# Kernel tuning notes

Measured on AMD Instinct MI355X. Metric: run time of the kernel, lower is better.

The kernel has to match this reference:

```python
import jax, jax.numpy as jnp
import numpy as np
import math

N_STFT = 1025
N_MELS = 128
SAMPLE_RATE = 16000
F_MIN = 0.0
F_MAX = 8000.0
MAX_ITER = 20
LR = 0.3
MOMENTUM = 0.9
BATCH = 4
TIME = 1024


def _create_fb_matrix(n_freqs, f_min, f_max, n_mels, sample_rate):
    # Triangular mel filterbank, (n_freqs, n_mels), matching torchaudio's create_fb_matrix.
    all_freqs = np.linspace(0.0, sample_rate // 2, n_freqs)
    m_min = 2595.0 * math.log10(1.0 + f_min / 700.0)
    m_max = 2595.0 * math.log10(1.0 + f_max / 700.0)
    m_pts = np.linspace(m_min, m_max, n_mels + 2)
    f_pts = 700.0 * (10.0 ** (m_pts / 2595.0) - 1.0)
    f_diff = f_pts[1:] - f_pts[:-1]
    slopes = f_pts[None, :] - all_freqs[:, None]  # (n_freqs, n_mels+2)
    down_slopes = -slopes[:, :-2] / f_diff[:-1]
    up_slopes = slopes[:, 2:] / f_diff[1:]
    fb = np.maximum(0.0, np.minimum(down_slopes, up_slopes))
    return jnp.asarray(fb, dtype=jnp.float32)


def setup_inputs() -> dict:
    key = jax.random.key(0)
    k1, k2 = jax.random.split(key)
    melspec = jax.random.uniform(k1, (BATCH, N_MELS, TIME), dtype=jnp.float32)
    # torch.rand initialization of the estimated spectrogram, exposed for determinism
    spec_init = jax.random.uniform(k2, (BATCH, TIME, N_STFT), dtype=jnp.float32)
    fb = _create_fb_matrix(N_STFT, F_MIN, F_MAX, N_MELS, SAMPLE_RATE)
    return {"melspec": melspec, "spec_init": spec_init, "fb": fb}


def reference(melspec, spec_init, fb):
    # melspec: (B, n_mels, T) -> (B, T, n_mels); fb: (n_stft, n_mels)
    mel_t = jnp.swapaxes(melspec, -1, -2)
    b, t, _ = mel_t.shape
    inv = 2.0 / (b * t)  # d(mean over B*T of sum_m diff^2)/d(spec) prefactor

    def step(carry, _):
        spec, buf = carry
        diff = mel_t - jnp.einsum('btf,fm->btm', spec, fb)      # (B,T,M)
        grad = -inv * jnp.einsum('btm,fm->btf', diff, fb)       # (B,T,F)
        buf = MOMENTUM * buf + grad                              # SGD momentum buffer
        spec = jnp.maximum(spec - LR * buf, 0.0)                 # update + clamp(min=0)
        return (spec, buf), None

    init = (spec_init, jnp.zeros_like(spec_init))
    (spec, _), _ = jax.lax.scan(step, init, None, length=MAX_ITER)
    return jnp.swapaxes(spec, -1, -2)  # (B, n_stft, T)
```

## Files before the change

kernel.cpp:

```cpp
#include <hip/hip_runtime.h>

#define N_STFT 1025
#define N_MELS 128
#define BATCH 4
#define TIME 1024
#define MAX_ITER 20

typedef unsigned int u32;

__global__ void imel_prep(const float* __restrict__ fb, int* __restrict__ m0f,
                          float* __restrict__ w0a, float* __restrict__ w1a) {
  const int w = threadIdx.x >> 6, l = threadIdx.x & 63;
  const int f = blockIdx.x * 4 + w;
  if (f >= N_STFT) return;
  const float* row = fb + (size_t)f * N_MELS;
  const unsigned long long mlo = __ballot(row[l] != 0.0f);
  const unsigned long long mhi = __ballot(row[l + 64] != 0.0f);
  if (l == 0) {
    int m0 = mlo ? __builtin_ctzll(mlo)
                 : (mhi ? 64 + __builtin_ctzll(mhi) : 0);
    if (m0 > N_MELS - 2) m0 = N_MELS - 2;
    m0f[f] = m0;
    w0a[f] = row[m0];
    w1a[f] = row[m0 + 1];
  }
}

__global__ __launch_bounds__(256, 4) void imel_main(
    const float* __restrict__ melspec, const float* __restrict__ spec_init,
    const int* __restrict__ m0f, const float* __restrict__ w0a,
    const float* __restrict__ w1a, float* __restrict__ out) {
  __shared__ u32   s_P[4][N_MELS];
  __shared__ float s_mel[4][N_MELS];
  __shared__ float s_out[4][1060];

  const int tid = threadIdx.x;
  const int w   = tid >> 6;
  const int l   = tid & 63;
  const int blk = blockIdx.x;
  const int b   = blk >> 8;
  const int t0  = (blk & 255) << 2;
  const int t   = t0 + w;

  for (int i = tid; i < 4 * N_MELS; i += 256) {
    const int m = i >> 2, r = i & 3;
    s_mel[r][m] = melspec[((size_t)b * N_MELS + m) * TIME + t0 + r];
  }
  __syncthreads();

  const float SCALE  = 16777216.0f;
  const float GRAD_N = -2.0f / (BATCH * TIME);
  const float C2 = (2.0f / (BATCH * TIME)) * 3.5527136788e-15f;

  float rs[16], rb[16], rw0[16], rw1[16], cc[16];
  int rm[16];

  const float* srow = spec_init + (size_t)(b * TIME + t) * N_STFT;
#pragma unroll
  for (int k = 0; k < 16; ++k) {
    const int f = (l << 4) + k;
    rs[k] = srow[f];
    const int m = m0f[f];
    rm[k] = m;
    const float w0 = w0a[f], w1 = w1a[f];
    rw0[k] = w0 * SCALE;
    rw1[k] = w1 * SCALE;
    cc[k]  = GRAD_N * fmaf(s_mel[w][m], w0, s_mel[w][m + 1] * w1);
    rb[k]  = 0.f;
  }
  const float rtail = (l == 63) ? srow[1024] : 0.f;

  bool adv[16];
  adv[0] = false;
#pragma unroll
  for (int k = 1; k < 16; ++k) adv[k] = (rm[k] != rm[k - 1]);

  u32* __restrict__ Pw = &s_P[w][0];
  Pw[l] = 0u;
  Pw[l + 64] = 0u;

  for (int it = 0; it < MAX_ITER; ++it) {
    {
      float a0 = rs[0] * rw0[0];
      float a1 = rs[0] * rw1[0];
#pragma unroll
      for (int k = 1; k < 16; ++k) {
        if (adv[k]) atomicAdd(&Pw[rm[k - 1]], (u32)__float2int_rn(a0));
        const float n0 = (adv[k] ? a1 : a0) + rs[k] * rw0[k];
        a1 = (adv[k] ? 0.f : a1) + rs[k] * rw1[k];
        a0 = n0;
      }
      atomicAdd(&Pw[rm[15]],     (u32)__float2int_rn(a0));
      atomicAdd(&Pw[rm[15] + 1], (u32)__float2int_rn(a1));
    }
    __builtin_amdgcn_wave_barrier();
    {
      float p0 = (float)(int)Pw[rm[0]];
      float p1 = (float)(int)Pw[rm[0] + 1];
#pragma unroll
      for (int k = 0; k < 16; ++k) {
        if (k > 0 && adv[k]) {
          p0 = p1;
          p1 = (float)(int)Pw[rm[k] + 1];
        }
        const float h = fmaf(p1, rw1[k], p0 * rw0[k]);
        const float g = fmaf(h, C2, cc[k]);
        rb[k] = fmaf(0.9f, rb[k], g);
        rs[k] = fmaxf(fmaf(-0.3f, rb[k], rs[k]), 0.f);
      }
    }
    __builtin_amdgcn_wave_barrier();
    Pw[l] = 0u;
    Pw[l + 64] = 0u;
    __builtin_amdgcn_wave_barrier();
  }

#pragma unroll
  for (int k = 0; k < 16; ++k) {
    const int f = (l << 4) + k;
    s_out[w][f + (f >> 5)] = rs[k];
  }
  if (l == 63) s_out[w][1056] = rtail;
  __syncthreads();

  const int tl = tid & 3;
  const int fg = tid >> 2;
  float* obase = out + (size_t)b * N_STFT * TIME + t0 + tl;
  for (int f = fg; f < N_STFT; f += 64) {
    obase[(size_t)f * TIME] = s_out[tl][f + (f >> 5)];
  }
}

extern "C" void kernel_launch(void* const* d_in, const int* in_sizes, int n_in,
                              void* d_out, int out_size, void* d_ws, size_t ws_size,
                              hipStream_t stream) {
  const float* melspec = (const float*)d_in[0];
  const float* spec_init = (const float*)d_in[1];
  const float* fb = (const float*)d_in[2];
  float* out = (float*)d_out;

  int* m0f = (int*)d_ws;
  float* w0a = (float*)((char*)d_ws + 5120);
  float* w1a = (float*)((char*)d_ws + 10240);

  imel_prep<<<dim3(257), dim3(256), 0, stream>>>(fb, m0f, w0a, w1a);
  imel_main<<<dim3(1024), dim3(256), 0, stream>>>(melspec, spec_init, m0f, w0a, w1a, out);
}
```

Baseline: 133.8 us.

## Process two time frames per wave with packed 64-bit LDS atomics

Each wave now handles two time frames instead of one. It packs the two frames' fixed-point partial sums into a single 64-bit LDS atomic, so the filterbank weights, mel indices and LDS atomics serve both frames. The grid is halved to 512 blocks, each covering 8 frames, with a swizzled block-to-(batch, time) mapping, and launch bounds drop to 2 blocks per CU to allow the extra registers. Halving LDS atomic and barrier overhead per frame costs higher register pressure and lower occupancy. Packing 32-bit integer lanes into a 64-bit add can carry from the low half into the high half when the low sum wraps.

Result: faster. 116.3 us (-13.1%).

```diff
diff --git a/kernel.cpp b/kernel.cpp
--- a/kernel.cpp
+++ b/kernel.cpp
@@ -6,6 +6,7 @@
 #define TIME 1024
 #define MAX_ITER 20
 
+typedef unsigned long long u64;
 typedef unsigned int u32;
 
 __global__ void imel_prep(const float* __restrict__ fb, int* __restrict__ m0f,
@@ -26,107 +27,126 @@
   }
 }
 
-__global__ __launch_bounds__(256, 4) void imel_main(
+__device__ __forceinline__ u64 pk_rn(float x, float y) {
+  return (u64)(u32)__float2int_rn(x) | ((u64)(u32)__float2int_rn(y) << 32);
+}
+
+__global__ __launch_bounds__(256, 2) void imel_main(
     const float* __restrict__ melspec, const float* __restrict__ spec_init,
     const int* __restrict__ m0f, const float* __restrict__ w0a,
     const float* __restrict__ w1a, float* __restrict__ out) {
-  __shared__ u32   s_P[4][N_MELS];
-  __shared__ float s_mel[4][N_MELS];
-  __shared__ float s_out[4][1060];
+  __shared__ u64   s_P[4][N_MELS];
+  __shared__ float s_mel[8][N_MELS];
+  __shared__ float s_out[8][1060];
 
   const int tid = threadIdx.x;
   const int w   = tid >> 6;
   const int l   = tid & 63;
-  const int blk = blockIdx.x;
-  const int b   = blk >> 8;
-  const int t0  = (blk & 255) << 2;
-  const int t   = t0 + w;
+  const int flat = (blockIdx.x & 7) * 64 + (blockIdx.x >> 3);
+  const int b   = flat >> 7;
+  const int t0  = (flat & 127) << 3;
+  const int tA  = t0 + 2 * w;
 
-  for (int i = tid; i < 4 * N_MELS; i += 256) {
-    const int m = i >> 2, r = i & 3;
+  for (int i = tid; i < 8 * N_MELS; i += 256) {
+    const int m = i >> 3, r = i & 7;
     s_mel[r][m] = melspec[((size_t)b * N_MELS + m) * TIME + t0 + r];
   }
   __syncthreads();
 
   const float SCALE  = 16777216.0f;
   const float GRAD_N = -2.0f / (BATCH * TIME);
-  const float C2 = (2.0f / (BATCH * TIME)) * 3.5527136788e-15f;
+  const float C2 = (2.0f / (BATCH * TIME)) * 3.5527136788005009e-15f;
 
-  float rs[16], rb[16], rw0[16], rw1[16], cc[16];
+  float rsA[16], rsB[16], rbA[16], rbB[16];
+  float rw0[16], rw1[16], ccA[16], ccB[16];
   int rm[16];
 
-  const float* srow = spec_init + (size_t)(b * TIME + t) * N_STFT;
+  const float* srowA = spec_init + (size_t)(b * TIME + tA) * N_STFT;
+  const float* srowB = srowA + N_STFT;
+  const float* melA = &s_mel[2 * w][0];
+  const float* melB = &s_mel[2 * w + 1][0];
 #pragma unroll
   for (int k = 0; k < 16; ++k) {
     const int f = (l << 4) + k;
-    rs[k] = srow[f];
+    rsA[k] = srowA[f];
+    rsB[k] = srowB[f];
     const int m = m0f[f];
     rm[k] = m;
     const float w0 = w0a[f], w1 = w1a[f];
     rw0[k] = w0 * SCALE;
     rw1[k] = w1 * SCALE;
-    cc[k]  = GRAD_N * fmaf(s_mel[w][m], w0, s_mel[w][m + 1] * w1);
-    rb[k]  = 0.f;
+    ccA[k] = GRAD_N * fmaf(melA[m], w0, melA[m + 1] * w1);
+    ccB[k] = GRAD_N * fmaf(melB[m], w0, melB[m + 1] * w1);
+    rbA[k] = 0.f;
+    rbB[k] = 0.f;
   }
-  const float rtail = (l == 63) ? srow[1024] : 0.f;
+  const float rtA = (l == 63) ? srowA[1024] : 0.f;
+  const float rtB = (l == 63) ? srowB[1024] : 0.f;
 
   bool adv[16];
   adv[0] = false;
 #pragma unroll
   for (int k = 1; k < 16; ++k) adv[k] = (rm[k] != rm[k - 1]);
 
-  u32* __restrict__ Pw = &s_P[w][0];
-  Pw[l] = 0u;
-  Pw[l + 64] = 0u;
+  u64* __restrict__ Pw = &s_P[w][0];
+  Pw[l] = 0ULL;
+  Pw[l + 64] = 0ULL;
 
   for (int it = 0; it < MAX_ITER; ++it) {
     {
-      float a0 = rs[0] * rw0[0];
-      float a1 = rs[0] * rw1[0];
+      float a0A = rsA[0] * rw0[0], a1A = rsA[0] * rw1[0];
+      float a0B = rsB[0] * rw0[0], a1B = rsB[0] * rw1[0];
 #pragma unroll
       for (int k = 1; k < 16; ++k) {
-        if (adv[k]) atomicAdd(&Pw[rm[k - 1]], (u32)__float2int_rn(a0));
-        const float n0 = (adv[k] ? a1 : a0) + rs[k] * rw0[k];
-        a1 = (adv[k] ? 0.f : a1) + rs[k] * rw1[k];
-        a0 = n0;
+        if (adv[k]) atomicAdd(&Pw[rm[k - 1]], pk_rn(a0A, a0B));
+        const float n0A = (adv[k] ? a1A : a0A) + rsA[k] * rw0[k];
+        a1A = (adv[k] ? 0.f : a1A) + rsA[k] * rw1[k];
+        a0A = n0A;
+        const float n0B = (adv[k] ? a1B : a0B) + rsB[k] * rw0[k];
+        a1B = (adv[k] ? 0.f : a1B) + rsB[k] * rw1[k];
+        a0B = n0B;
       }
-      atomicAdd(&Pw[rm[15]],     (u32)__float2int_rn(a0));
-      atomicAdd(&Pw[rm[15] + 1], (u32)__float2int_rn(a1));
+      atomicAdd(&Pw[rm[15]],     pk_rn(a0A, a0B));
+      atomicAdd(&Pw[rm[15] + 1], pk_rn(a1A, a1B));
     }
     __builtin_amdgcn_wave_barrier();
-    {
-      float p0 = (float)(int)Pw[rm[0]];
-      float p1 = (float)(int)Pw[rm[0] + 1];
 #pragma unroll
-      for (int k = 0; k < 16; ++k) {
-        if (k > 0 && adv[k]) {
-          p0 = p1;
-          p1 = (float)(int)Pw[rm[k] + 1];
-        }
-        const float h = fmaf(p1, rw1[k], p0 * rw0[k]);
-        const float g = fmaf(h, C2, cc[k]);
-        rb[k] = fmaf(0.9f, rb[k], g);
-        rs[k] = fmaxf(fmaf(-0.3f, rb[k], rs[k]), 0.f);
-      }
+    for (int k = 0; k < 16; ++k) {
+      const u64 q0 = Pw[rm[k]];
+      const u64 q1 = Pw[rm[k] + 1];
+      const float p0A = (float)(int)(u32)q0;
+      const float p0B = (float)(int)(u32)(q0 >> 32);
+      const float p1A = (float)(int)(u32)q1;
+      const float p1B = (float)(int)(u32)(q1 >> 32);
+      const float gA = fmaf(fmaf(p1A, rw1[k], p0A * rw0[k]), C2, ccA[k]);
+      const float gB = fmaf(fmaf(p1B, rw1[k], p0B * rw0[k]), C2, ccB[k]);
+      rbA[k] = fmaf(0.9f, rbA[k], gA);
+      rbB[k] = fmaf(0.9f, rbB[k], gB);
+      rsA[k] = fmaxf(fmaf(-0.3f, rbA[k], rsA[k]), 0.f);
+      rsB[k] = fmaxf(fmaf(-0.3f, rbB[k], rsB[k]), 0.f);
     }
     __builtin_amdgcn_wave_barrier();
-    Pw[l] = 0u;
-    Pw[l + 64] = 0u;
+    Pw[l] = 0ULL;
+    Pw[l + 64] = 0ULL;
     __builtin_amdgcn_wave_barrier();
   }
 
 #pragma unroll
   for (int k = 0; k < 16; ++k) {
     const int f = (l << 4) + k;
-    s_out[w][f + (f >> 5)] = rs[k];
+    s_out[2 * w][f + (f >> 5)]     = rsA[k];
+    s_out[2 * w + 1][f + (f >> 5)] = rsB[k];
   }
-  if (l == 63) s_out[w][1056] = rtail;
+  if (l == 63) {
+    s_out[2 * w][1056]     = rtA;
+    s_out[2 * w + 1][1056] = rtB;
+  }
   __syncthreads();
 
-  const int tl = tid & 3;
-  const int fg = tid >> 2;
+  const int tl = tid & 7;
+  const int fg = tid >> 3;
   float* obase = out + (size_t)b * N_STFT * TIME + t0 + tl;
-  for (int f = fg; f < N_STFT; f += 64) {
+  for (int f = fg; f < N_STFT; f += 32) {
     obase[(size_t)f * TIME] = s_out[tl][f + (f >> 5)];
   }
 }
@@ -144,5 +164,5 @@
   float* w1a = (float*)((char*)d_ws + 10240);
 
   imel_prep<<<dim3(257), dim3(256), 0, stream>>>(fb, m0f, w0a, w1a);
-  imel_main<<<dim3(1024), dim3(256), 0, stream>>>(melspec, spec_init, m0f, w0a, w1a, out);
+  imel_main<<<dim3(512), dim3(256), 0, stream>>>(melspec, spec_init, m0f, w0a, w1a, out);
 }
```
